# Kernel optimization log

Hardware: AMD Instinct MI355X
Metric: run time of the kernel (lower is better)

Reference implementation:

```python
import jax, jax.numpy as jnp
import numpy as np

N_NODES = 50000
N_EDGES = 800000
IN_CH = 128
HIDDEN = 32
HEADS = 4
NEG_SLOPE = 0.2


def segment_softmax(e, seg, num_segments):
    # numerically stable softmax over edges grouped by destination node
    m = jax.ops.segment_max(e, seg, num_segments=num_segments)
    ex = jnp.exp(e - m[seg])
    denom = jax.ops.segment_sum(ex, seg, num_segments=num_segments)
    return ex / denom[seg]


def gat_layer(x, src, dst, W, a_src, a_dst, b, num_nodes, concat):
    H, C = a_src.shape
    h = (x @ W).reshape(num_nodes, H, C)            # (N, H, C)
    alpha_s = jnp.einsum('nhc,hc->nh', h, a_src)    # (N, H)
    alpha_d = jnp.einsum('nhc,hc->nh', h, a_dst)    # (N, H)
    e = jax.nn.leaky_relu(alpha_s[src] + alpha_d[dst], negative_slope=NEG_SLOPE)  # (E, H)
    att = segment_softmax(e, dst, num_nodes)        # (E, H)
    out = jax.ops.segment_sum(h[src] * att[:, :, None], dst, num_segments=num_nodes)  # (N, H, C)
    if concat:
        out = out.reshape(num_nodes, H * C)
    else:
        out = out.mean(axis=1)
    return out + b


def setup_inputs() -> dict:
    key = jax.random.key(0)
    ks = jax.random.split(key, 12)
    s = 0.1
    return {
        'x': jax.random.normal(ks[0], (N_NODES, IN_CH), dtype=jnp.float32),
        'edge_index': jax.random.randint(ks[1], (2, N_EDGES), 0, N_NODES, dtype=jnp.int64),
        'W1': jax.random.normal(ks[2], (IN_CH, HEADS * HIDDEN), dtype=jnp.float32) * s,
        'a_src1': jax.random.normal(ks[3], (HEADS, HIDDEN), dtype=jnp.float32) * s,
        'a_dst1': jax.random.normal(ks[4], (HEADS, HIDDEN), dtype=jnp.float32) * s,
        'b1': jnp.zeros((HEADS * HIDDEN,), dtype=jnp.float32),
        'W2': jax.random.normal(ks[5], (HEADS * HIDDEN, 1 * HIDDEN), dtype=jnp.float32) * s,
        'a_src2': jax.random.normal(ks[6], (1, HIDDEN), dtype=jnp.float32) * s,
        'a_dst2': jax.random.normal(ks[7], (1, HIDDEN), dtype=jnp.float32) * s,
        'b2': jnp.zeros((HIDDEN,), dtype=jnp.float32),
    }


def reference(x, edge_index, W1, a_src1, a_dst1, b1, W2, a_src2, a_dst2, b2):
    n = x.shape[0]
    loops = jnp.arange(n, dtype=edge_index.dtype)
    src = jnp.concatenate([edge_index[0], loops])  # PyG GATConv add_self_loops=True
    dst = jnp.concatenate([edge_index[1], loops])
    h = gat_layer(x, src, dst, W1, a_src1, a_dst1, b1, n, concat=True)
    h = jax.nn.elu(h)  # ELU between layers (dropout=0.0)
    out = gat_layer(h, src, dst, W2, a_src2, a_dst2, b2, n, concat=False)
    return out
```

## Files before the change

kernel.cpp:

```cpp
#include <hip/hip_runtime.h>
#include <cstdint>

#define NEG_SLOPE 0.2f
#define LDA 136
#define HB  256
#define CAP 5120
#define SMEM_BYTES (64 * LDA * 2)

__device__ __forceinline__ float leaky(float v) { return v > 0.f ? v : NEG_SLOPE * v; }
__device__ __forceinline__ float elu(float v) { return v > 0.f ? v : __expf(v) - 1.f; }

typedef _Float16 half2v __attribute__((ext_vector_type(2)));
typedef _Float16 f16x8 __attribute__((ext_vector_type(8)));
typedef float f32x4 __attribute__((ext_vector_type(4)));
union H8 { float4 f4; half2v h[4]; f16x8 v8; };
union H4 { float2 f2; half2v h[2]; };
union HF2 { float2 f2; _Float16 h[4]; };
union HH { f16x8 v; half2v h[4]; };


__device__ __forceinline__ void prep_body(int bid, int G, int tid,
        const float* __restrict__ W1, const float* __restrict__ W2,
        _Float16* __restrict__ W1t, _Float16* __restrict__ W2t) {
    for (int i = bid * 256 + tid; i < 128 * 128; i += G * 256) {
        int c = i >> 7, k = i & 127;
        W1t[i] = (_Float16)W1[k * 128 + c];
    }
    for (int i = bid * 256 + tid; i < 32 * 128; i += G * 256) {
        int c = i >> 7, k = i & 127;
        W2t[i] = (_Float16)W2[k * 32 + c];
    }
}

__device__ __forceinline__ void hist_chunk(int c, int tid, int* lh,
        const int* __restrict__ dstp, int* __restrict__ hist, int E, int NB, int CH) {
    for (int t = tid; t < NB; t += 256) lh[t] = 0;
    __syncthreads();
    int e0 = c * CH, e1 = min(e0 + CH, E);
    int nv = (e1 - e0) & ~3;
    for (int i = e0 + tid * 4; i < e0 + nv; i += 1024) {
        int4 d = *(const int4*)(dstp + i);
        atomicAdd(&lh[d.x >> 8], 1);
        atomicAdd(&lh[d.y >> 8], 1);
        atomicAdd(&lh[d.z >> 8], 1);
        atomicAdd(&lh[d.w >> 8], 1);
    }
    for (int i = e0 + nv + tid; i < e1; i += 256)
        atomicAdd(&lh[dstp[i] >> 8], 1);
    __syncthreads();
    for (int t = tid; t < NB; t += 256) hist[t * HB + c] = lh[t];
}

__device__ __forceinline__ void pair_chunk(int c, int tid, int* lcur,
        const int* __restrict__ src, const int* __restrict__ dstp,
        const int* __restrict__ hist, int2* __restrict__ pairs,
        int E, int NB, int CH) {
    for (int b = tid; b < NB; b += 256) {
        const int4* row = (const int4*)(hist + b * HB);
        int s = 0;
        int c4 = c >> 2;
#pragma unroll 4
        for (int i = 0; i < c4; ++i) { int4 v = row[i]; s += v.x + v.y + v.z + v.w; }
        for (int i = c4 * 4; i < c; ++i) s += hist[b * HB + i];
        lcur[b] = s;
    }
    __syncthreads();
    int e0 = c * CH, e1 = min(e0 + CH, E);
    int nv = (e1 - e0) & ~3;
    for (int i = e0 + tid * 4; i < e0 + nv; i += 1024) {
        int4 d = *(const int4*)(dstp + i);
        int4 s = *(const int4*)(src + i);
        int b0 = d.x >> 8, b1 = d.y >> 8, b2 = d.z >> 8, b3 = d.w >> 8;
        int r0 = atomicAdd(&lcur[b0], 1);
        int r1 = atomicAdd(&lcur[b1], 1);
        int r2 = atomicAdd(&lcur[b2], 1);
        int r3 = atomicAdd(&lcur[b3], 1);
        if (r0 < CAP) pairs[(size_t)b0 * CAP + r0] = make_int2(s.x, d.x & 255);
        if (r1 < CAP) pairs[(size_t)b1 * CAP + r1] = make_int2(s.y, d.y & 255);
        if (r2 < CAP) pairs[(size_t)b2 * CAP + r2] = make_int2(s.z, d.z & 255);
        if (r3 < CAP) pairs[(size_t)b3 * CAP + r3] = make_int2(s.w, d.w & 255);
    }
    for (int i = e0 + nv + tid; i < e1; i += 256) {
        int d = dstp[i];
        int b = d >> 8;
        int r = atomicAdd(&lcur[b], 1);
        if (r < CAP) pairs[(size_t)b * CAP + r] = make_int2(src[i], d & 255);
    }
}

__device__ __forceinline__ void gemm1_tile(int b, int tid, _Float16* Ah,
        const float* __restrict__ x, const _Float16* __restrict__ W1t,
        const float* __restrict__ a_src, const float* __restrict__ a_dst,
        _Float16* __restrict__ h1h, float* __restrict__ as1, float* __restrict__ ad1,
        int n) {
    int row0 = b * 64;
    const float4* x4 = (const float4*)x;
#pragma unroll
    for (int i = 0; i < 8; ++i) {
        int idx = tid + i * 256;
        int row = idx >> 5, c4 = idx & 31;
        float4 v = make_float4(0.f, 0.f, 0.f, 0.f);
        if (row0 + row < n) v = x4[(size_t)(row0 + row) * 32 + c4];
        HF2 u;
        u.h[0] = (_Float16)v.x; u.h[1] = (_Float16)v.y;
        u.h[2] = (_Float16)v.z; u.h[3] = (_Float16)v.w;
        *(float2*)&Ah[row * LDA + c4 * 4] = u.f2;
    }
    __syncthreads();

    int l = tid & 63, w = tid >> 6;
    int lr = l & 15, lg = l >> 4;
    f16x8 af[4];
#pragma unroll
    for (int kk = 0; kk < 4; ++kk)
        af[kk] = *(const f16x8*)&Ah[(w * 16 + lr) * LDA + kk * 32 + lg * 8];
    f32x4 acc[8];
#pragma unroll
    for (int t = 0; t < 8; ++t) acc[t] = (f32x4)0.f;
#pragma unroll
    for (int t = 0; t < 8; ++t) {
#pragma unroll
        for (int kk = 0; kk < 4; ++kk) {
            f16x8 bf = *(const f16x8*)&W1t[(size_t)(t * 16 + lr) * 128 + kk * 32 + lg * 8];
            acc[t] = __builtin_amdgcn_mfma_f32_16x16x32_f16(af[kk], bf, acc[t], 0, 0, 0);
        }
    }
    __syncthreads();
#pragma unroll
    for (int t = 0; t < 8; ++t)
#pragma unroll
        for (int r = 0; r < 4; ++r)
            Ah[(w * 16 + lg * 4 + r) * LDA + t * 16 + lr] = (_Float16)acc[t][r];
    __syncthreads();
    int row = tid >> 2, q = tid & 3;
    if (row0 + row < n) {
        const float* asv = a_src + q * 32;
        const float* adv = a_dst + q * 32;
        float ps = 0.f, pd = 0.f;
#pragma unroll
        for (int j = 0; j < 4; ++j) {
            f16x8 v = *(const f16x8*)&Ah[row * LDA + q * 32 + j * 8];
            *(f16x8*)&h1h[(size_t)(row0 + row) * 128 + q * 32 + j * 8] = v;
#pragma unroll
            for (int e = 0; e < 8; ++e) {
                float f = (float)v[e];
                ps += f * asv[j * 8 + e];
                pd += f * adv[j * 8 + e];
            }
        }
        as1[(row0 + row) * 4 + q] = ps;
        ad1[(row0 + row) * 4 + q] = pd;
    }
}

__device__ __forceinline__ void csr_bucket(int b, int tid, unsigned char* smem,
        const int2* __restrict__ pairs, const int* __restrict__ hist,
        int* __restrict__ rp, int* __restrict__ col, int E, int N, int NB) {
    int* lsz    = (int*)smem;
    int* lstart = lsz + 256;
    int* lnh    = lstart + 256;
    int* lnex   = lnh + 256;
    int* lncur  = lnex + 256;
    int* wsum   = lncur + 256;
    int* woff   = wsum + 4;
    int lane = tid & 63, wv = tid >> 6;

    {
        int s = 0;
        if (tid < NB) {
            const int4* row = (const int4*)(hist + tid * HB);
#pragma unroll 8
            for (int i = 0; i < HB / 4; ++i) { int4 v = row[i]; s += v.x + v.y + v.z + v.w; }
        }
        lsz[tid] = s;
    }
    __syncthreads();
    int v = lsz[tid];
    int x = v;
#pragma unroll
    for (int o = 1; o < 64; o <<= 1) { int u = __shfl_up(x, o); if (lane >= o) x += u; }
    if (lane == 63) wsum[wv] = x;
    __syncthreads();
    if (tid == 0) { int a = 0; for (int i = 0; i < 4; ++i) { woff[i] = a; a += wsum[i]; } }
    __syncthreads();
    lstart[tid] = x - v + woff[wv];
    __syncthreads();

    if (b >= NB) { if (tid == 0) rp[N] = E; return; }
    int myStart = lstart[b];
    int S = lsz[b]; if (S > CAP) S = CAP;
    const int2* pb = pairs + (size_t)b * CAP;

    lnh[tid] = 0;
    __syncthreads();
    for (int i = tid; i < S; i += 256) atomicAdd(&lnh[pb[i].y], 1);
    __syncthreads();
    int v2 = lnh[tid];
    int x2 = v2;
#pragma unroll
    for (int o = 1; o < 64; o <<= 1) { int u = __shfl_up(x2, o); if (lane >= o) x2 += u; }
    if (lane == 63) wsum[wv] = x2;
    __syncthreads();
    if (tid == 0) { int a = 0; for (int i = 0; i < 4; ++i) { woff[i] = a; a += wsum[i]; } }
    __syncthreads();
    int ex2 = x2 - v2 + woff[wv];
    lnex[tid] = ex2;
    lncur[tid] = 0;
    int node = (b << 8) + tid;
    if (node <= N) rp[node] = myStart + ex2;
    __syncthreads();
    for (int i = tid; i < S; i += 256) {
        int2 p = pb[i];
        int r = atomicAdd(&lncur[p.y], 1);
        col[myStart + lnex[p.y] + r] = p.x;
    }
}


__global__ __launch_bounds__(256) void prep_hist_kernel(
        const float* __restrict__ W1, const float* __restrict__ W2,
        _Float16* __restrict__ W1t, _Float16* __restrict__ W2t,
        const int* __restrict__ dstp, int* __restrict__ hist, int E, int NB, int CH) {
    __shared__ int lh[256];
    int bid = (int)blockIdx.x;
    if (bid < HB) {
        hist_chunk(bid, threadIdx.x, lh, dstp, hist, E, NB, CH);
        return;
    }
    prep_body(bid - HB, (int)gridDim.x - HB, threadIdx.x, W1, W2, W1t, W2t);
}

__global__ __launch_bounds__(256) void pair_kernel(const int* __restrict__ src,
                                                   const int* __restrict__ dstp,
                                                   const int* __restrict__ hist,
                                                   int2* __restrict__ pairs,
                                                   int E, int NB, int CH) {
    __shared__ int lcur[256];
    pair_chunk(blockIdx.x, threadIdx.x, lcur, src, dstp, hist, pairs, E, NB, CH);
}

__global__ __launch_bounds__(256) void csr_gemm_kernel(
        const int2* __restrict__ pairs, const int* __restrict__ hist,
        int* __restrict__ rp, int* __restrict__ col, int E, int N, int NB, int KB,
        const float* __restrict__ x, const _Float16* __restrict__ W1t,
        const float* __restrict__ a_src, const float* __restrict__ a_dst,
        _Float16* __restrict__ h1h, float* __restrict__ as1, float* __restrict__ ad1) {
    __shared__ __align__(16) unsigned char smem[SMEM_BYTES];
    int bid = (int)blockIdx.x;
    if (bid < KB) {
        csr_bucket(bid, threadIdx.x, smem, pairs, hist, rp, col, E, N, NB);
        return;
    }
    gemm1_tile(bid - KB, threadIdx.x, (_Float16*)smem, x, W1t, a_src, a_dst,
               h1h, as1, ad1, N);
}

#define W2S 136

__global__ __launch_bounds__(256) void agg1_kernel(const _Float16* __restrict__ h1h,
                                                   const float4* __restrict__ as1,
                                                   const float4* __restrict__ ad1,
                                                   const int* __restrict__ rp,
                                                   const int* __restrict__ col,
                                                   const float* __restrict__ b1,
                                                   const _Float16* __restrict__ W2t,
                                                   const float* __restrict__ a_src2,
                                                   const float* __restrict__ a_dst2,
                                                   _Float16* __restrict__ h2h,
                                                   float* __restrict__ as2,
                                                   float* __restrict__ ad2, int n) {
    __shared__ float4 s_p[4][64];
    __shared__ _Float16 s_row[4][128];
    __shared__ _Float16 sW2[32 * W2S];
    int tid = threadIdx.x;
    for (int e = tid; e < 32 * 16; e += 256) {
        int c = e >> 4, k8 = e & 15;
        *(f16x8*)&sW2[c * W2S + k8 * 8] = *(const f16x8*)&W2t[c * 128 + k8 * 8];
    }
    float a2s = a_src2[tid & 31], a2d = a_dst2[tid & 31];
    __syncthreads();

    int wave = tid >> 6, lane = tid & 63;
    int nid = blockIdx.x * 4 + wave;
    if (nid >= n) return;
    float4* sp = s_p[wave];
    int start = rp[nid], end = rp[nid + 1];
    float4 adn = ad1[nid], asn = as1[nid];
    int g = lane & 15, sub = lane >> 4;
    int head = g >> 2;
    float sv = (head == 0) ? asn.x + adn.x : (head == 1) ? asn.y + adn.y
             : (head == 2) ? asn.z + adn.z : asn.w + adn.w;
    float psf_h = __expf(leaky(sv));
    float dnum = 0.f;
    float4 a0 = make_float4(0.f, 0.f, 0.f, 0.f);
    float4 a1 = a0;

    for (int base = start; base < end; base += 64) {
        int i = base + lane;
        int sidx = 0;
        float4 p = make_float4(0.f, 0.f, 0.f, 0.f);
        if (i < end) {
            sidx = col[i];
            float4 a = as1[sidx];
            p.x = __expf(leaky(a.x + adn.x));
            p.y = __expf(leaky(a.y + adn.y));
            p.z = __expf(leaky(a.z + adn.z));
            p.w = __expf(leaky(a.w + adn.w));
        }
        sp[lane] = p;
        int len = min(64, end - base);
        int steps = (len + 3) >> 2;
#pragma unroll 4
        for (int s = 0; s < steps; ++s) {
            int j = s * 4 + sub;
            bool valid = j < len;
            int js = valid ? j : 0;
            int rj = __shfl(sidx, js);
            float pj = ((const float*)&sp[js])[head];
            pj = valid ? pj : 0.f;
            H8 u = ((const H8*)(h1h + (size_t)rj * 128))[g];
            dnum += pj;
            a0.x += (float)u.h[0].x * pj; a0.y += (float)u.h[0].y * pj;
            a0.z += (float)u.h[1].x * pj; a0.w += (float)u.h[1].y * pj;
            a1.x += (float)u.h[2].x * pj; a1.y += (float)u.h[2].y * pj;
            a1.z += (float)u.h[3].x * pj; a1.w += (float)u.h[3].y * pj;
        }
    }
    if (sub == 0) {
        H8 u = ((const H8*)(h1h + (size_t)nid * 128))[g];
        dnum += psf_h;
        a0.x += (float)u.h[0].x * psf_h; a0.y += (float)u.h[0].y * psf_h;
        a0.z += (float)u.h[1].x * psf_h; a0.w += (float)u.h[1].y * psf_h;
        a1.x += (float)u.h[2].x * psf_h; a1.y += (float)u.h[2].y * psf_h;
        a1.z += (float)u.h[3].x * psf_h; a1.w += (float)u.h[3].y * psf_h;
    }
#pragma unroll
    for (int o = 16; o < 64; o <<= 1) {
        a0.x += __shfl_xor(a0.x, o); a0.y += __shfl_xor(a0.y, o);
        a0.z += __shfl_xor(a0.z, o); a0.w += __shfl_xor(a0.w, o);
        a1.x += __shfl_xor(a1.x, o); a1.y += __shfl_xor(a1.y, o);
        a1.z += __shfl_xor(a1.z, o); a1.w += __shfl_xor(a1.w, o);
        dnum += __shfl_xor(dnum, o);
    }
    if (sub == 0) {
        float inv = __builtin_amdgcn_rcpf(dnum);
        const float4* b4 = (const float4*)b1;
        float4 bb0 = b4[g * 2], bb1 = b4[g * 2 + 1];
        float4 r0 = make_float4(elu(a0.x * inv + bb0.x), elu(a0.y * inv + bb0.y),
                                elu(a0.z * inv + bb0.z), elu(a0.w * inv + bb0.w));
        float4 r1 = make_float4(elu(a1.x * inv + bb1.x), elu(a1.y * inv + bb1.y),
                                elu(a1.z * inv + bb1.z), elu(a1.w * inv + bb1.w));
        H8 o8;
        o8.h[0] = half2v{(_Float16)r0.x, (_Float16)r0.y};
        o8.h[1] = half2v{(_Float16)r0.z, (_Float16)r0.w};
        o8.h[2] = half2v{(_Float16)r1.x, (_Float16)r1.y};
        o8.h[3] = half2v{(_Float16)r1.z, (_Float16)r1.w};
        *(float4*)&s_row[wave][g * 8] = o8.f4;
    }
    int c = lane & 31, half = lane >> 5;
    float acc2 = 0.f;
#pragma unroll
    for (int k8 = 0; k8 < 8; ++k8) {
        HH rv, wvv;
        rv.v  = *(const f16x8*)&s_row[wave][half * 64 + k8 * 8];
        wvv.v = *(const f16x8*)&sW2[c * W2S + half * 64 + k8 * 8];
#if __has_builtin(__builtin_amdgcn_fdot2)
        acc2 = __builtin_amdgcn_fdot2(rv.h[0], wvv.h[0], acc2, false);
        acc2 = __builtin_amdgcn_fdot2(rv.h[1], wvv.h[1], acc2, false);
        acc2 = __builtin_amdgcn_fdot2(rv.h[2], wvv.h[2], acc2, false);
        acc2 = __builtin_amdgcn_fdot2(rv.h[3], wvv.h[3], acc2, false);
#else
#pragma unroll
        for (int e = 0; e < 8; ++e) acc2 += (float)rv.v[e] * (float)wvv.v[e];
#endif
    }
    acc2 += __shfl_xor(acc2, 32);
    float ps = acc2 * a2s, pd = acc2 * a2d;
#pragma unroll
    for (int o = 1; o < 32; o <<= 1) { ps += __shfl_xor(ps, o); pd += __shfl_xor(pd, o); }
    if (lane < 32) h2h[(size_t)nid * 32 + c] = (_Float16)acc2;
    if (lane == 0) { as2[nid] = ps; ad2[nid] = pd; }
}

__global__ __launch_bounds__(256) void agg2_kernel(const _Float16* __restrict__ h2h,
                                                   const float* __restrict__ as2,
                                                   const float* __restrict__ ad2,
                                                   const int* __restrict__ rp,
                                                   const int* __restrict__ col,
                                                   const float* __restrict__ b2,
                                                   float* __restrict__ out, int n) {
    int wave = threadIdx.x >> 6, lane = threadIdx.x & 63;
    int nid = blockIdx.x * 4 + wave;
    if (nid >= n) return;
    int start = rp[nid], end = rp[nid + 1];
    float adn = ad2[nid];
    float psf = __expf(leaky(as2[nid] + adn));
    int g = lane & 7, sub = lane >> 3;
    float dnum = 0.f;
    float4 acc = make_float4(0.f, 0.f, 0.f, 0.f);
    for (int base = start; base < end; base += 64) {
        int i = base + lane;
        int sidx = 0;
        float p = 0.f;
        if (i < end) {
            sidx = col[i];
            p = __expf(leaky(as2[sidx] + adn));
        }
        int len = min(64, end - base);
        int steps = (len + 7) >> 3;
#pragma unroll 4
        for (int s = 0; s < steps; ++s) {
            int j = s * 8 + sub;
            bool valid = j < len;
            int js = valid ? j : 0;
            int rj = __shfl(sidx, js);
            float pj = __shfl(p, js);
            pj = valid ? pj : 0.f;
            H4 u = ((const H4*)(h2h + (size_t)rj * 32))[g];
            dnum += pj;
            acc.x += (float)u.h[0].x * pj; acc.y += (float)u.h[0].y * pj;
            acc.z += (float)u.h[1].x * pj; acc.w += (float)u.h[1].y * pj;
        }
    }
    if (sub == 0) {
        H4 u = ((const H4*)(h2h + (size_t)nid * 32))[g];
        dnum += psf;
        acc.x += (float)u.h[0].x * psf; acc.y += (float)u.h[0].y * psf;
        acc.z += (float)u.h[1].x * psf; acc.w += (float)u.h[1].y * psf;
    }
#pragma unroll
    for (int o = 8; o < 64; o <<= 1) {
        acc.x += __shfl_xor(acc.x, o); acc.y += __shfl_xor(acc.y, o);
        acc.z += __shfl_xor(acc.z, o); acc.w += __shfl_xor(acc.w, o);
        dnum += __shfl_xor(dnum, o);
    }
    if (sub == 0) {
        float inv = __builtin_amdgcn_rcpf(dnum);
        float4 bb = ((const float4*)b2)[g];
        ((float4*)(out + (size_t)nid * 32))[g] =
            make_float4(acc.x * inv + bb.x, acc.y * inv + bb.y,
                        acc.z * inv + bb.z, acc.w * inv + bb.w);
    }
}


extern "C" void kernel_launch(void* const* d_in, const int* in_sizes, int n_in,
                              void* d_out, int out_size, void* d_ws, size_t ws_size,
                              hipStream_t stream) {
    const float* x      = (const float*)d_in[0];
    const int*   ei     = (const int*)d_in[1];
    const float* W1     = (const float*)d_in[2];
    const float* a_src1 = (const float*)d_in[3];
    const float* a_dst1 = (const float*)d_in[4];
    const float* b1     = (const float*)d_in[5];
    const float* W2     = (const float*)d_in[6];
    const float* a_src2 = (const float*)d_in[7];
    const float* a_dst2 = (const float*)d_in[8];
    const float* b2     = (const float*)d_in[9];
    float* out = (float*)d_out;

    const int N = in_sizes[0] / 128;
    const int E = in_sizes[1] / 2;
    const int* src = ei;
    const int* dstp = ei + E;

    uint8_t* w = (uint8_t*)d_ws;
    auto carve = [&](size_t bytes) {
        uint8_t* p = w;
        w += (bytes + 255) & ~(size_t)255;
        return p;
    };
    _Float16* h1h = (_Float16*)carve((size_t)N * 128 * 2);
    _Float16* h2h = (_Float16*)carve((size_t)N * 32 * 2);
    _Float16* W1t = (_Float16*)carve((size_t)128 * 128 * 2);
    _Float16* W2t = (_Float16*)carve((size_t)32 * 128 * 2);
    float* as1 = (float*)carve((size_t)N * 4 * 4);
    float* ad1 = (float*)carve((size_t)N * 4 * 4);
    float* as2 = (float*)carve((size_t)N * 4);
    float* ad2 = (float*)carve((size_t)N * 4);
    int* rp    = (int*)carve((size_t)(N + 1) * 4);
    int* col   = (int*)carve((size_t)E * 4);
    int* hist  = (int*)carve((size_t)256 * HB * 4);

    const int NB = ((N - 1) >> 8) + 1;
    const int KB = (N >> 8) + 1;
    int CH = (E + HB - 1) / HB;
    CH = (CH + 3) & ~3;
    const int gemmBlocks = (N + 63) / 64;
    const int aggGroups = (N + 3) / 4;

    int2* pairs = (int2*)carve((size_t)NB * CAP * 8);

    prep_hist_kernel<<<HB + 80, 256, 0, stream>>>(W1, W2, W1t, W2t, dstp, hist, E, NB, CH);
    pair_kernel<<<HB, 256, 0, stream>>>(src, dstp, hist, pairs, E, NB, CH);
    csr_gemm_kernel<<<KB + gemmBlocks, 256, 0, stream>>>(
        pairs, hist, rp, col, E, N, NB, KB,
        x, W1t, a_src1, a_dst1, h1h, as1, ad1);
    agg1_kernel<<<aggGroups, 256, 0, stream>>>(h1h, (const float4*)as1,
                                               (const float4*)ad1, rp, col, b1,
                                               W2t, a_src2, a_dst2, h2h, as2, ad2, N);
    agg2_kernel<<<aggGroups, 256, 0, stream>>>(h2h, as2, ad2, rp, col, b2, out, N);
}
```

Measured before the change: 205.5 us.

## Process two destination nodes per wave in both aggregation kernels

Each 64-lane wave now splits into two 32-lane halves, and each half aggregates a separate destination node in agg1 and agg2. The average degree is about 17, so a 64-edge chunk left most lanes idle during the exp and gather phase; halving the chunk width is meant to raise lane utilisation and halve the grid. In agg1 the fused W2 projection now has each half-wave do a full 128-long dot product per output channel instead of splitting K across halves. The trade-off is fewer neighbours gathered in parallel per node, more loop iterations for high-degree nodes, and a longer serial dot product.

```diff
diff --git a/kernel.cpp b/kernel.cpp
--- a/kernel.cpp
+++ b/kernel.cpp
@@ -270,7 +270,7 @@
                                                    float* __restrict__ as2,
                                                    float* __restrict__ ad2, int n) {
     __shared__ float4 s_p[4][64];
-    __shared__ _Float16 s_row[4][128];
+    __shared__ _Float16 s_row[4][2][128];
     __shared__ _Float16 sW2[32 * W2S];
     int tid = threadIdx.x;
     for (int e = tid; e < 32 * 16; e += 256) {
@@ -281,22 +281,25 @@
     __syncthreads();
 
     int wave = tid >> 6, lane = tid & 63;
-    int nid = blockIdx.x * 4 + wave;
-    if (nid >= n) return;
+    int h = lane >> 5, l5 = lane & 31;
+    int g = l5 & 15, sub = l5 >> 4;
+    int head = g >> 2;
+    int nid = blockIdx.x * 8 + wave * 2 + h;
+    bool vn = nid < n;
+    int nc = vn ? nid : 0;
     float4* sp = s_p[wave];
-    int start = rp[nid], end = rp[nid + 1];
-    float4 adn = ad1[nid], asn = as1[nid];
-    int g = lane & 15, sub = lane >> 4;
-    int head = g >> 2;
+    int start = rp[nc];
+    int end = vn ? rp[nc + 1] : start;
+    float4 adn = ad1[nc], asn = as1[nc];
     float sv = (head == 0) ? asn.x + adn.x : (head == 1) ? asn.y + adn.y
              : (head == 2) ? asn.z + adn.z : asn.w + adn.w;
-    float psf_h = __expf(leaky(sv));
+    float psf_h = vn ? __expf(leaky(sv)) : 0.f;
     float dnum = 0.f;
     float4 a0 = make_float4(0.f, 0.f, 0.f, 0.f);
     float4 a1 = a0;
 
-    for (int base = start; base < end; base += 64) {
-        int i = base + lane;
+    for (int base = start; base < end; base += 32) {
+        int i = base + l5;
         int sidx = 0;
         float4 p = make_float4(0.f, 0.f, 0.f, 0.f);
         if (i < end) {
@@ -308,15 +311,16 @@
             p.w = __expf(leaky(a.w + adn.w));
         }
         sp[lane] = p;
-        int len = min(64, end - base);
-        int steps = (len + 3) >> 2;
+        int len = min(32, end - base);
+        int steps = (len + 1) >> 1;
 #pragma unroll 4
         for (int s = 0; s < steps; ++s) {
-            int j = s * 4 + sub;
+            int j = s * 2 + sub;
             bool valid = j < len;
             int js = valid ? j : 0;
-            int rj = __shfl(sidx, js);
-            float pj = ((const float*)&sp[js])[head];
+            int sl = (h << 5) + js;
+            int rj = __shfl(sidx, sl);
+            float pj = ((const float*)&sp[sl])[head];
             pj = valid ? pj : 0.f;
             H8 u = ((const H8*)(h1h + (size_t)rj * 128))[g];
             dnum += pj;
@@ -327,22 +331,19 @@
         }
     }
     if (sub == 0) {
-        H8 u = ((const H8*)(h1h + (size_t)nid * 128))[g];
+        H8 u = ((const H8*)(h1h + (size_t)nc * 128))[g];
         dnum += psf_h;
         a0.x += (float)u.h[0].x * psf_h; a0.y += (float)u.h[0].y * psf_h;
         a0.z += (float)u.h[1].x * psf_h; a0.w += (float)u.h[1].y * psf_h;
         a1.x += (float)u.h[2].x * psf_h; a1.y += (float)u.h[2].y * psf_h;
         a1.z += (float)u.h[3].x * psf_h; a1.w += (float)u.h[3].y * psf_h;
     }
-#pragma unroll
-    for (int o = 16; o < 64; o <<= 1) {
-        a0.x += __shfl_xor(a0.x, o); a0.y += __shfl_xor(a0.y, o);
-        a0.z += __shfl_xor(a0.z, o); a0.w += __shfl_xor(a0.w, o);
-        a1.x += __shfl_xor(a1.x, o); a1.y += __shfl_xor(a1.y, o);
-        a1.z += __shfl_xor(a1.z, o); a1.w += __shfl_xor(a1.w, o);
-        dnum += __shfl_xor(dnum, o);
-    }
-    if (sub == 0) {
+    a0.x += __shfl_xor(a0.x, 16); a0.y += __shfl_xor(a0.y, 16);
+    a0.z += __shfl_xor(a0.z, 16); a0.w += __shfl_xor(a0.w, 16);
+    a1.x += __shfl_xor(a1.x, 16); a1.y += __shfl_xor(a1.y, 16);
+    a1.z += __shfl_xor(a1.z, 16); a1.w += __shfl_xor(a1.w, 16);
+    dnum += __shfl_xor(dnum, 16);
+    if (sub == 0 && vn) {
         float inv = __builtin_amdgcn_rcpf(dnum);
         const float4* b4 = (const float4*)b1;
         float4 bb0 = b4[g * 2], bb1 = b4[g * 2 + 1];
@@ -355,15 +356,15 @@
         o8.h[1] = half2v{(_Float16)r0.z, (_Float16)r0.w};
         o8.h[2] = half2v{(_Float16)r1.x, (_Float16)r1.y};
         o8.h[3] = half2v{(_Float16)r1.z, (_Float16)r1.w};
-        *(float4*)&s_row[wave][g * 8] = o8.f4;
-    }
-    int c = lane & 31, half = lane >> 5;
+        *(float4*)&s_row[wave][h][g * 8] = o8.f4;
+    }
+    int c = l5;
     float acc2 = 0.f;
 #pragma unroll
-    for (int k8 = 0; k8 < 8; ++k8) {
+    for (int k8 = 0; k8 < 16; ++k8) {
         HH rv, wvv;
-        rv.v  = *(const f16x8*)&s_row[wave][half * 64 + k8 * 8];
-        wvv.v = *(const f16x8*)&sW2[c * W2S + half * 64 + k8 * 8];
+        rv.v  = *(const f16x8*)&s_row[wave][h][k8 * 8];
+        wvv.v = *(const f16x8*)&sW2[c * W2S + k8 * 8];
 #if __has_builtin(__builtin_amdgcn_fdot2)
         acc2 = __builtin_amdgcn_fdot2(rv.h[0], wvv.h[0], acc2, false);
         acc2 = __builtin_amdgcn_fdot2(rv.h[1], wvv.h[1], acc2, false);
@@ -374,12 +375,13 @@
         for (int e = 0; e < 8; ++e) acc2 += (float)rv.v[e] * (float)wvv.v[e];
 #endif
     }
-    acc2 += __shfl_xor(acc2, 32);
     float ps = acc2 * a2s, pd = acc2 * a2d;
 #pragma unroll
     for (int o = 1; o < 32; o <<= 1) { ps += __shfl_xor(ps, o); pd += __shfl_xor(pd, o); }
-    if (lane < 32) h2h[(size_t)nid * 32 + c] = (_Float16)acc2;
-    if (lane == 0) { as2[nid] = ps; ad2[nid] = pd; }
+    if (vn) {
+        h2h[(size_t)nid * 32 + c] = (_Float16)acc2;
+        if (l5 == 0) { as2[nid] = ps; ad2[nid] = pd; }
+    }
 }
 
 __global__ __launch_bounds__(256) void agg2_kernel(const _Float16* __restrict__ h2h,
@@ -390,31 +392,35 @@
                                                    const float* __restrict__ b2,
                                                    float* __restrict__ out, int n) {
     int wave = threadIdx.x >> 6, lane = threadIdx.x & 63;
-    int nid = blockIdx.x * 4 + wave;
-    if (nid >= n) return;
-    int start = rp[nid], end = rp[nid + 1];
-    float adn = ad2[nid];
-    float psf = __expf(leaky(as2[nid] + adn));
-    int g = lane & 7, sub = lane >> 3;
+    int h = lane >> 5, l5 = lane & 31;
+    int g = l5 & 7, sub = l5 >> 3;
+    int nid = blockIdx.x * 8 + wave * 2 + h;
+    bool vn = nid < n;
+    int nc = vn ? nid : 0;
+    int start = rp[nc];
+    int end = vn ? rp[nc + 1] : start;
+    float adn = ad2[nc];
+    float psf = vn ? __expf(leaky(as2[nc] + adn)) : 0.f;
     float dnum = 0.f;
     float4 acc = make_float4(0.f, 0.f, 0.f, 0.f);
-    for (int base = start; base < end; base += 64) {
-        int i = base + lane;
+    for (int base = start; base < end; base += 32) {
+        int i = base + l5;
         int sidx = 0;
         float p = 0.f;
         if (i < end) {
             sidx = col[i];
             p = __expf(leaky(as2[sidx] + adn));
         }
-        int len = min(64, end - base);
-        int steps = (len + 7) >> 3;
+        int len = min(32, end - base);
+        int steps = (len + 3) >> 2;
 #pragma unroll 4
         for (int s = 0; s < steps; ++s) {
-            int j = s * 8 + sub;
+            int j = s * 4 + sub;
             bool valid = j < len;
             int js = valid ? j : 0;
-            int rj = __shfl(sidx, js);
-            float pj = __shfl(p, js);
+            int sl = (h << 5) + js;
+            int rj = __shfl(sidx, sl);
+            float pj = __shfl(p, sl);
             pj = valid ? pj : 0.f;
             H4 u = ((const H4*)(h2h + (size_t)rj * 32))[g];
             dnum += pj;
@@ -423,18 +429,18 @@
         }
     }
     if (sub == 0) {
-        H4 u = ((const H4*)(h2h + (size_t)nid * 32))[g];
+        H4 u = ((const H4*)(h2h + (size_t)nc * 32))[g];
         dnum += psf;
         acc.x += (float)u.h[0].x * psf; acc.y += (float)u.h[0].y * psf;
         acc.z += (float)u.h[1].x * psf; acc.w += (float)u.h[1].y * psf;
     }
 #pragma unroll
-    for (int o = 8; o < 64; o <<= 1) {
+    for (int o = 8; o < 32; o <<= 1) {
         acc.x += __shfl_xor(acc.x, o); acc.y += __shfl_xor(acc.y, o);
         acc.z += __shfl_xor(acc.z, o); acc.w += __shfl_xor(acc.w, o);
         dnum += __shfl_xor(dnum, o);
     }
-    if (sub == 0) {
+    if (sub == 0 && vn) {
         float inv = __builtin_amdgcn_rcpf(dnum);
         float4 bb = ((const float4*)b2)[g];
         ((float4*)(out + (size_t)nid * 32))[g] =
@@ -487,7 +493,7 @@
     int CH = (E + HB - 1) / HB;
     CH = (CH + 3) & ~3;
     const int gemmBlocks = (N + 63) / 64;
-    const int aggGroups = (N + 3) / 4;
+    const int aggGroups = (N + 7) / 8;
 
     int2* pairs = (int2*)carve((size_t)NB * CAP * 8);
 
```

Result: faster. 193.1 us (-6.0%).
